# Optimization experiments

Measured on AMD Instinct MI355X. Metric: run time of the kernel, lower is better.

## Reference

```python
import jax, jax.numpy as jnp
import numpy as np

B, NQ, NK, D, H = 4, 512, 512, 128, 32  # batch, n_queries, n_keys, kq_size, mlp hidden


def setup_inputs() -> dict:
    key = jax.random.key(0)
    ks = jax.random.split(key, 7)
    s_in = 1.0 / np.sqrt(2 * D)
    s_h = 1.0 / np.sqrt(H)
    return {
        "keys": jax.random.normal(ks[0], (B, NK, D), dtype=jnp.float32),
        "queries": jax.random.normal(ks[1], (B, NQ, D), dtype=jnp.float32),
        # first MLP layer Linear(2D, H) split into key-half and query-half
        "Wk": jax.random.uniform(ks[2], (D, H), jnp.float32, -s_in, s_in),
        "Wq": jax.random.uniform(ks[3], (D, H), jnp.float32, -s_in, s_in),
        "b1": jax.random.uniform(ks[4], (H,), jnp.float32, -s_in, s_in),
        # second MLP layer Linear(H, 1)
        "w2": jax.random.uniform(ks[5], (H,), jnp.float32, -s_h, s_h),
        "b2": jax.random.uniform(ks[6], (), jnp.float32, -s_h, s_h),
    }


def reference(keys, queries, Wk, Wq, b1, w2, b2):
    # AdditiveScorer: logits[b,q,k] = w2 . tanh(W1 @ [keys[b,k]; queries[b,q]] + b1) + b2
    # Split the concat-linear into two GEMMs (identical math, no [B,Q,K,2D] tensor).
    kh = jnp.einsum("bkd,dh->bkh", keys, Wk)            # (B, NK, H)
    qh = jnp.einsum("bqd,dh->bqh", queries, Wq)          # (B, NQ, H)
    h = jnp.tanh(qh[:, :, None, :] + kh[:, None, :, :] + b1)  # (B, NQ, NK, H)
    logits = jnp.einsum("bqkh,h->bqk", h, w2) + b2       # (B, NQ, NK)
    attn = jax.nn.softmax(logits, axis=-1)               # softmax over keys
    context = jnp.einsum("bqk,bkd->bqd", attn, keys)     # weighted value sum (values = keys)
    return context
```

## Files before the change

kernel.cpp:

```cpp
#include <hip/hip_runtime.h>

#define B 4
#define NQ 512
#define NK 512
#define D 128
#define H 32
#define G 4
#define PS 2.8853900817779268f

__device__ __forceinline__ float rcp_f(float x)  { return __builtin_amdgcn_rcpf(x); }
__device__ __forceinline__ float exp2_f(float x) { return __builtin_amdgcn_exp2f(x); }

__device__ __forceinline__ void fma4(float4& a, const float4& v, float s) {
    a.x = fmaf(s, v.x, a.x);
    a.y = fmaf(s, v.y, a.y);
    a.z = fmaf(s, v.z, a.z);
    a.w = fmaf(s, v.w, a.w);
}

__global__ __launch_bounds__(256) void proj_kernel(
    const float* __restrict__ keys, const float* __restrict__ queries,
    const float* __restrict__ Wk, const float* __restrict__ Wq,
    const float* __restrict__ b1,
    float* __restrict__ kh_t, float* __restrict__ qh)
{
    __shared__ float xs[8][D];
    const int tid = threadIdx.x;
    const int r0 = blockIdx.x * 8;
    const bool is_q = (r0 >= B * NK);
    const float* __restrict__ X = is_q ? (queries + (size_t)(r0 - B * NK) * D)
                                       : (keys + (size_t)r0 * D);
    const float* __restrict__ W = is_q ? Wq : Wk;

    reinterpret_cast<float4*>(&xs[0][0])[tid] =
        reinterpret_cast<const float4*>(X)[tid];
    __syncthreads();

    const int lr = tid >> 5;
    const int h  = tid & 31;
    float a0 = 0.f, a1 = 0.f, a2 = 0.f, a3 = 0.f;
    const float4* x4 = reinterpret_cast<const float4*>(&xs[lr][0]);
    #pragma unroll
    for (int i = 0; i < D / 4; ++i) {
        float4 v = x4[i];
        a0 = fmaf(v.x, W[(4 * i + 0) * H + h], a0);
        a1 = fmaf(v.y, W[(4 * i + 1) * H + h], a1);
        a2 = fmaf(v.z, W[(4 * i + 2) * H + h], a2);
        a3 = fmaf(v.w, W[(4 * i + 3) * H + h], a3);
    }
    float acc = (a0 + a1) + (a2 + a3);
    if (is_q) {
        const int rq = r0 - B * NK + lr;
        qh[(size_t)rq * H + h] = acc * PS;
    } else {
        const int r = r0 + lr;
        const int b = r >> 9;
        const int k = r & (NK - 1);
        kh_t[((size_t)b * H + h) * NK + k] = (acc + b1[h]) * PS;
    }
}

__global__ __launch_bounds__(256) void attend_kernel(
    const float* __restrict__ keys,
    const float* __restrict__ kh_t,
    const float* __restrict__ qh,
    const float* __restrict__ w2,
    float* __restrict__ outp)
{
    __shared__ float ex_t[G][NK];
    __shared__ float acc_s[8][G][D];
    __shared__ float qv_s[G][H];
    __shared__ float w2_s[H];

    const int tid  = threadIdx.x;
    const int lane = tid & 63;
    const int w    = tid >> 6;
    const int b    = blockIdx.x >> 7;
    const int q0   = (blockIdx.x & 127) * G;

    if (lane < H) {
        qv_s[w][lane] = qh[((size_t)b * NQ + q0 + w) * H + lane];
        if (w == 0) w2_s[lane] = -PS * w2[lane];
    }
    __syncthreads();

    float l[8];
    #pragma unroll
    for (int j = 0; j < 8; ++j) l[j] = 0.f;
    const float* khb = kh_t + (size_t)b * H * NK;
    #pragma unroll 8
    for (int h = 0; h < H; ++h) {
        const float4 v0 = reinterpret_cast<const float4*>(khb + h * NK)[lane];
        const float4 v1 = reinterpret_cast<const float4*>(khb + h * NK + 256)[lane];
        const float qv = qv_s[w][h];
        const float wp = w2_s[h];
        l[0] = fmaf(wp, rcp_f(1.f + exp2_f(qv + v0.x)), l[0]);
        l[1] = fmaf(wp, rcp_f(1.f + exp2_f(qv + v0.y)), l[1]);
        l[2] = fmaf(wp, rcp_f(1.f + exp2_f(qv + v0.z)), l[2]);
        l[3] = fmaf(wp, rcp_f(1.f + exp2_f(qv + v0.w)), l[3]);
        l[4] = fmaf(wp, rcp_f(1.f + exp2_f(qv + v1.x)), l[4]);
        l[5] = fmaf(wp, rcp_f(1.f + exp2_f(qv + v1.y)), l[5]);
        l[6] = fmaf(wp, rcp_f(1.f + exp2_f(qv + v1.z)), l[6]);
        l[7] = fmaf(wp, rcp_f(1.f + exp2_f(qv + v1.w)), l[7]);
    }

    float m = l[0];
    #pragma unroll
    for (int j = 1; j < 8; ++j) m = fmaxf(m, l[j]);
    #pragma unroll
    for (int off = 32; off; off >>= 1) m = fmaxf(m, __shfl_xor(m, off));
    float e[8], s = 0.f;
    #pragma unroll
    for (int j = 0; j < 8; ++j) { e[j] = exp2_f(l[j] - m); s += e[j]; }
    #pragma unroll
    for (int off = 32; off; off >>= 1) s += __shfl_xor(s, off);
    const float inv = 1.f / s;
    const float4 st0 = { e[0] * inv, e[1] * inv, e[2] * inv, e[3] * inv };
    const float4 st1 = { e[4] * inv, e[5] * inv, e[6] * inv, e[7] * inv };
    reinterpret_cast<float4*>(&ex_t[w][0])[lane]   = st0;
    reinterpret_cast<float4*>(&ex_t[w][256])[lane] = st1;
    __syncthreads();

    const int dg = tid & 31;
    const int kp = tid >> 5;
    const float4* k4 = reinterpret_cast<const float4*>(
        keys + ((size_t)b * NK + kp * 64) * D) + dg;
    float4 a0 = {0,0,0,0}, a1 = a0, a2 = a0, a3 = a0;
    #pragma unroll 8
    for (int kk = 0; kk < 64; ++kk) {
        float4 kv = k4[(size_t)kk * (D / 4)];
        const int k = kp * 64 + kk;
        fma4(a0, kv, ex_t[0][k]);
        fma4(a1, kv, ex_t[1][k]);
        fma4(a2, kv, ex_t[2][k]);
        fma4(a3, kv, ex_t[3][k]);
    }
    *reinterpret_cast<float4*>(&acc_s[kp][0][4 * dg]) = a0;
    *reinterpret_cast<float4*>(&acc_s[kp][1][4 * dg]) = a1;
    *reinterpret_cast<float4*>(&acc_s[kp][2][4 * dg]) = a2;
    *reinterpret_cast<float4*>(&acc_s[kp][3][4 * dg]) = a3;
    __syncthreads();

    const int o = 2 * tid;
    const int g = o >> 7;
    const int d = o & 127;
    float2 r = {0.f, 0.f};
    #pragma unroll
    for (int p = 0; p < 8; ++p) {
        float2 v = *reinterpret_cast<const float2*>(&acc_s[p][g][d]);
        r.x += v.x; r.y += v.y;
    }
    *reinterpret_cast<float2*>(&outp[((size_t)b * NQ + q0 + g) * D + d]) = r;
}

extern "C" void kernel_launch(void* const* d_in, const int* in_sizes, int n_in,
                              void* d_out, int out_size, void* d_ws, size_t ws_size,
                              hipStream_t stream) {
    const float* keys    = (const float*)d_in[0];
    const float* queries = (const float*)d_in[1];
    const float* Wk      = (const float*)d_in[2];
    const float* Wq      = (const float*)d_in[3];
    const float* b1      = (const float*)d_in[4];
    const float* w2      = (const float*)d_in[5];
    float* out = (float*)d_out;

    float* kh_t = (float*)d_ws;
    float* qh   = kh_t + (size_t)B * H * NK;

    const int proj_blocks = (B * NK + B * NQ) / 8;
    proj_kernel<<<proj_blocks, 256, 0, stream>>>(keys, queries, Wk, Wq, b1, kh_t, qh);
    attend_kernel<<<B * NQ / G, 256, 0, stream>>>(keys, kh_t, qh, w2, out);
}
```

Measured before the change: 23.41 us.

## Split attend kernel into separate score/softmax and context kernels via workspace

The fused attend kernel is split into a score kernel that computes the tanh-MLP logits and softmax for two queries per block and writes normalized probabilities to global workspace, and a context kernel with 512 threads that reads those probabilities and accumulates the weighted key sum over 16 key partitions. The aim is to rebalance parallelism and register pressure between the transcendental-heavy scoring phase and the memory-bound weighted-sum phase. The cost is an extra launch and a global write and read of the B*NQ*NK probability matrix, about 4 MB.

```diff
diff --git a/kernel.cpp b/kernel.cpp
--- a/kernel.cpp
+++ b/kernel.cpp
@@ -60,80 +60,105 @@
     }
 }
 
-__global__ __launch_bounds__(256) void attend_kernel(
-    const float* __restrict__ keys,
+__global__ __launch_bounds__(256) void score_kernel(
     const float* __restrict__ kh_t,
     const float* __restrict__ qh,
     const float* __restrict__ w2,
+    float* __restrict__ ex)
+{
+    __shared__ float qv_s[2][H];
+    __shared__ float w2_s[H];
+    __shared__ float redm[2][4];
+    __shared__ float reds[2][4];
+
+    const int tid = threadIdx.x;
+    const int w   = tid >> 6;
+    const int b   = blockIdx.x >> 8;
+    const int q0  = (blockIdx.x & 255) * 2;
+
+    if (tid < H)            w2_s[tid] = -PS * w2[tid];
+    else if (tid < 2 * H)   qv_s[0][tid - H]     = qh[((size_t)b * NQ + q0) * H + (tid - H)];
+    else if (tid < 3 * H)   qv_s[1][tid - 2 * H] = qh[((size_t)b * NQ + q0 + 1) * H + (tid - 2 * H)];
+    __syncthreads();
+
+    const float* khb = kh_t + (size_t)b * H * NK;
+    float l00 = 0.f, l01 = 0.f, l10 = 0.f, l11 = 0.f;
+    #pragma unroll 8
+    for (int h = 0; h < H; ++h) {
+        const float2 kv = *reinterpret_cast<const float2*>(khb + h * NK + 2 * tid);
+        const float qv0 = qv_s[0][h];
+        const float qv1 = qv_s[1][h];
+        const float wp  = w2_s[h];
+        l00 = fmaf(wp, rcp_f(1.f + exp2_f(qv0 + kv.x)), l00);
+        l01 = fmaf(wp, rcp_f(1.f + exp2_f(qv0 + kv.y)), l01);
+        l10 = fmaf(wp, rcp_f(1.f + exp2_f(qv1 + kv.x)), l10);
+        l11 = fmaf(wp, rcp_f(1.f + exp2_f(qv1 + kv.y)), l11);
+    }
+
+    float m0 = fmaxf(l00, l01), m1 = fmaxf(l10, l11);
+    #pragma unroll
+    for (int off = 32; off; off >>= 1) {
+        m0 = fmaxf(m0, __shfl_xor(m0, off));
+        m1 = fmaxf(m1, __shfl_xor(m1, off));
+    }
+    if ((tid & 63) == 0) { redm[0][w] = m0; redm[1][w] = m1; }
+    __syncthreads();
+    m0 = fmaxf(fmaxf(redm[0][0], redm[0][1]), fmaxf(redm[0][2], redm[0][3]));
+    m1 = fmaxf(fmaxf(redm[1][0], redm[1][1]), fmaxf(redm[1][2], redm[1][3]));
+
+    const float e00 = exp2_f(l00 - m0), e01 = exp2_f(l01 - m0);
+    const float e10 = exp2_f(l10 - m1), e11 = exp2_f(l11 - m1);
+    float s0 = e00 + e01, s1 = e10 + e11;
+    #pragma unroll
+    for (int off = 32; off; off >>= 1) {
+        s0 += __shfl_xor(s0, off);
+        s1 += __shfl_xor(s1, off);
+    }
+    if ((tid & 63) == 0) { reds[0][w] = s0; reds[1][w] = s1; }
+    __syncthreads();
+    s0 = (reds[0][0] + reds[0][1]) + (reds[0][2] + reds[0][3]);
+    s1 = (reds[1][0] + reds[1][1]) + (reds[1][2] + reds[1][3]);
+    const float inv0 = 1.f / s0, inv1 = 1.f / s1;
+
+    const float2 o0 = { e00 * inv0, e01 * inv0 };
+    const float2 o1 = { e10 * inv1, e11 * inv1 };
+    reinterpret_cast<float2*>(ex + ((size_t)b * NQ + q0) * NK)[tid]     = o0;
+    reinterpret_cast<float2*>(ex + ((size_t)b * NQ + q0 + 1) * NK)[tid] = o1;
+}
+
+__global__ __launch_bounds__(512) void context_kernel(
+    const float* __restrict__ keys,
+    const float* __restrict__ ex,
     float* __restrict__ outp)
 {
-    __shared__ float ex_t[G][NK];
-    __shared__ float acc_s[8][G][D];
-    __shared__ float qv_s[G][H];
-    __shared__ float w2_s[H];
+    __shared__ float acc_s[16][G][D];
 
-    const int tid  = threadIdx.x;
-    const int lane = tid & 63;
-    const int w    = tid >> 6;
-    const int b    = blockIdx.x >> 7;
-    const int q0   = (blockIdx.x & 127) * G;
+    const int tid = threadIdx.x;
+    const int dg  = tid & 31;
+    const int kp  = tid >> 5;
+    const int b   = blockIdx.x >> 7;
+    const int q0  = (blockIdx.x & 127) * G;
 
-    if (lane < H) {
-        qv_s[w][lane] = qh[((size_t)b * NQ + q0 + w) * H + lane];
-        if (w == 0) w2_s[lane] = -PS * w2[lane];
-    }
-    __syncthreads();
+    const float4* k4 = reinterpret_cast<const float4*>(
+        keys + ((size_t)b * NK + kp * 32) * D) + dg;
+    const float* exb = ex + ((size_t)b * NQ + q0) * NK + kp * 32;
 
-    float l[8];
-    #pragma unroll
-    for (int j = 0; j < 8; ++j) l[j] = 0.f;
-    const float* khb = kh_t + (size_t)b * H * NK;
-    #pragma unroll 8
-    for (int h = 0; h < H; ++h) {
-        const float4 v0 = reinterpret_cast<const float4*>(khb + h * NK)[lane];
-        const float4 v1 = reinterpret_cast<const float4*>(khb + h * NK + 256)[lane];
-        const float qv = qv_s[w][h];
-        const float wp = w2_s[h];
-        l[0] = fmaf(wp, rcp_f(1.f + exp2_f(qv + v0.x)), l[0]);
-        l[1] = fmaf(wp, rcp_f(1.f + exp2_f(qv + v0.y)), l[1]);
-        l[2] = fmaf(wp, rcp_f(1.f + exp2_f(qv + v0.z)), l[2]);
-        l[3] = fmaf(wp, rcp_f(1.f + exp2_f(qv + v0.w)), l[3]);
-        l[4] = fmaf(wp, rcp_f(1.f + exp2_f(qv + v1.x)), l[4]);
-        l[5] = fmaf(wp, rcp_f(1.f + exp2_f(qv + v1.y)), l[5]);
-        l[6] = fmaf(wp, rcp_f(1.f + exp2_f(qv + v1.z)), l[6]);
-        l[7] = fmaf(wp, rcp_f(1.f + exp2_f(qv + v1.w)), l[7]);
-    }
-
-    float m = l[0];
-    #pragma unroll
-    for (int j = 1; j < 8; ++j) m = fmaxf(m, l[j]);
-    #pragma unroll
-    for (int off = 32; off; off >>= 1) m = fmaxf(m, __shfl_xor(m, off));
-    float e[8], s = 0.f;
-    #pragma unroll
-    for (int j = 0; j < 8; ++j) { e[j] = exp2_f(l[j] - m); s += e[j]; }
-    #pragma unroll
-    for (int off = 32; off; off >>= 1) s += __shfl_xor(s, off);
-    const float inv = 1.f / s;
-    const float4 st0 = { e[0] * inv, e[1] * inv, e[2] * inv, e[3] * inv };
-    const float4 st1 = { e[4] * inv, e[5] * inv, e[6] * inv, e[7] * inv };
-    reinterpret_cast<float4*>(&ex_t[w][0])[lane]   = st0;
-    reinterpret_cast<float4*>(&ex_t[w][256])[lane] = st1;
-    __syncthreads();
-
-    const int dg = tid & 31;
-    const int kp = tid >> 5;
-    const float4* k4 = reinterpret_cast<const float4*>(
-        keys + ((size_t)b * NK + kp * 64) * D) + dg;
     float4 a0 = {0,0,0,0}, a1 = a0, a2 = a0, a3 = a0;
-    #pragma unroll 8
-    for (int kk = 0; kk < 64; ++kk) {
-        float4 kv = k4[(size_t)kk * (D / 4)];
-        const int k = kp * 64 + kk;
-        fma4(a0, kv, ex_t[0][k]);
-        fma4(a1, kv, ex_t[1][k]);
-        fma4(a2, kv, ex_t[2][k]);
-        fma4(a3, kv, ex_t[3][k]);
+    #pragma unroll 2
+    for (int kk4 = 0; kk4 < 8; ++kk4) {
+        float ev0[4], ev1[4], ev2[4], ev3[4];
+        *reinterpret_cast<float4*>(ev0) = reinterpret_cast<const float4*>(exb)[kk4];
+        *reinterpret_cast<float4*>(ev1) = reinterpret_cast<const float4*>(exb + NK)[kk4];
+        *reinterpret_cast<float4*>(ev2) = reinterpret_cast<const float4*>(exb + 2 * NK)[kk4];
+        *reinterpret_cast<float4*>(ev3) = reinterpret_cast<const float4*>(exb + 3 * NK)[kk4];
+        #pragma unroll
+        for (int j = 0; j < 4; ++j) {
+            float4 kv = k4[(size_t)(4 * kk4 + j) * (D / 4)];
+            fma4(a0, kv, ev0[j]);
+            fma4(a1, kv, ev1[j]);
+            fma4(a2, kv, ev2[j]);
+            fma4(a3, kv, ev3[j]);
+        }
     }
     *reinterpret_cast<float4*>(&acc_s[kp][0][4 * dg]) = a0;
     *reinterpret_cast<float4*>(&acc_s[kp][1][4 * dg]) = a1;
@@ -141,16 +166,12 @@
     *reinterpret_cast<float4*>(&acc_s[kp][3][4 * dg]) = a3;
     __syncthreads();
 
-    const int o = 2 * tid;
-    const int g = o >> 7;
-    const int d = o & 127;
-    float2 r = {0.f, 0.f};
+    const int g = tid >> 7;
+    const int d = tid & 127;
+    float r = 0.f;
     #pragma unroll
-    for (int p = 0; p < 8; ++p) {
-        float2 v = *reinterpret_cast<const float2*>(&acc_s[p][g][d]);
-        r.x += v.x; r.y += v.y;
-    }
-    *reinterpret_cast<float2*>(&outp[((size_t)b * NQ + q0 + g) * D + d]) = r;
+    for (int p = 0; p < 16; ++p) r += acc_s[p][g][d];
+    outp[((size_t)b * NQ + q0 + g) * D + d] = r;
 }
 
 extern "C" void kernel_launch(void* const* d_in, const int* in_sizes, int n_in,
@@ -166,8 +187,9 @@
 
     float* kh_t = (float*)d_ws;
     float* qh   = kh_t + (size_t)B * H * NK;
+    float* exw  = qh + (size_t)B * NQ * H;
 
-    const int proj_blocks = (B * NK + B * NQ) / 8;
-    proj_kernel<<<proj_blocks, 256, 0, stream>>>(keys, queries, Wk, Wq, b1, kh_t, qh);
-    attend_kernel<<<B * NQ / G, 256, 0, stream>>>(keys, kh_t, qh, w2, out);
+    proj_kernel<<<(B * NK + B * NQ) / 8, 256, 0, stream>>>(keys, queries, Wk, Wq, b1, kh_t, qh);
+    score_kernel<<<B * NQ / 2, 256, 0, stream>>>(kh_t, qh, w2, exw);
+    context_kernel<<<B * NQ / G, 512, 0, stream>>>(keys, exw, out);
 }
```

Measured after the change: 30.18 us. 1.29x slower.
